# Optimization experiments

Measured on AMD Instinct MI355X. Metric: run time of the kernel, lower is better.

The kernel has to match this reference:

```python
import jax, jax.numpy as jnp
import numpy as np

N = 100000
E = 1600000
IN_DIM = 128
HEADS = 8
OUT_PER_HEAD = 16  # output_dim // heads = 128 // 8
NEG_SLOPE = 0.2    # PyG GATConv default negative_slope


def setup_inputs() -> dict:
    key = jax.random.key(0)
    k_x, k_ei, k_w, k_as, k_ad, k_b = jax.random.split(key, 6)
    x = jax.random.normal(k_x, (N, IN_DIM), dtype=jnp.float32)
    edge_index = jax.random.randint(k_ei, (2, E), 0, N, dtype=jnp.int64)
    # GATConv params (Glorot-ish scale)
    scale = 1.0 / np.sqrt(IN_DIM)
    W = jax.random.normal(k_w, (IN_DIM, HEADS, OUT_PER_HEAD), dtype=jnp.float32) * scale
    a_src = jax.random.normal(k_as, (HEADS, OUT_PER_HEAD), dtype=jnp.float32) * scale
    a_dst = jax.random.normal(k_ad, (HEADS, OUT_PER_HEAD), dtype=jnp.float32) * scale
    bias = jnp.zeros((HEADS * OUT_PER_HEAD,), dtype=jnp.float32)
    return {"x": x, "edge_index": edge_index, "W": W, "a_src": a_src,
            "a_dst": a_dst, "bias": bias}


def reference(x, edge_index, W, a_src, a_dst, bias):
    # Linear projection per head: [N, H, F]
    xp = jnp.einsum('ni,ihf->nhf', x, W)
    # Per-node attention halves: [N, H]
    al_src = jnp.einsum('nhf,hf->nh', xp, a_src)
    al_dst = jnp.einsum('nhf,hf->nh', xp, a_dst)
    src, dst = edge_index[0], edge_index[1]
    # Edge logits with LeakyReLU: [E, H]
    e = al_src[src] + al_dst[dst]
    e = jnp.where(e >= 0, e, NEG_SLOPE * e)
    # Segment softmax over incoming edges of each dst node
    m = jnp.full((N, HEADS), -jnp.inf, dtype=e.dtype).at[dst].max(e)
    ex = jnp.exp(e - m[dst])
    denom = jnp.zeros((N, HEADS), dtype=e.dtype).at[dst].add(ex)
    alpha = ex / jnp.where(denom[dst] == 0, 1.0, denom[dst])  # [E, H]
    # Weighted scatter-aggregate of source messages: [N, H, F]
    out = jnp.zeros((N, HEADS, OUT_PER_HEAD), dtype=xp.dtype)
    out = out.at[dst].add(xp[src] * alpha[:, :, None])
    # Concat heads, bias, ELU (GATLayer applies F.elu)
    out = out.reshape(N, HEADS * OUT_PER_HEAD) + bias
    return jnp.where(out > 0, out, jnp.expm1(out))
```

## Files before the change

kernel.cpp:

```cpp
#include <hip/hip_runtime.h>
#include <hip/hip_fp16.h>
#include <cstdint>

constexpr int IN_DIM = 128;
constexpr int OUT_DIM = 128;
constexpr int HEADS = 8;
constexpr float NEG_SLOPE = 0.2f;

constexpr int BUCKET_CAP = 5120;
constexpr int BIN_TILE   = 4096;

typedef _Float16 f16x8 __attribute__((ext_vector_type(8)));
typedef float    f32x4 __attribute__((ext_vector_type(4)));

__global__ __launch_bounds__(256) void proj_kernel(
    const float* __restrict__ x, const float* __restrict__ W,
    __half* __restrict__ xp, int N)
{
  __shared__ __half xs[64 * 128];
  __shared__ __half Wt[128 * 128];
  const int t  = threadIdx.x;
  const int r0 = blockIdx.x * 64;

#pragma unroll
  for (int it = 0; it < 4; ++it) {
    int m   = t + it * 256;
    int row = m >> 4;
    int g   = m & 15;
    int grow = r0 + row;
    float4 v0 = make_float4(0.f,0.f,0.f,0.f), v1 = v0;
    if (grow < N) {
      const float* src = &x[(size_t)grow * IN_DIM + g * 8];
      v0 = *(const float4*)src;
      v1 = *(const float4*)(src + 4);
    }
    union { __half2 h2[4]; uint4 u; } u;
    u.h2[0] = __floats2half2_rn(v0.x, v0.y);
    u.h2[1] = __floats2half2_rn(v0.z, v0.w);
    u.h2[2] = __floats2half2_rn(v1.x, v1.y);
    u.h2[3] = __floats2half2_rn(v1.z, v1.w);
    *(uint4*)&xs[row * 128 + ((g ^ (row & 15)) << 3)] = u.u;
  }
#pragma unroll
  for (int it = 0; it < 16; ++it) {
    int m  = t + it * 256;
    int c  = m & 127;
    int kq = m >> 7;
    int k  = kq * 4;
    float w0 = W[(size_t)(k + 0) * OUT_DIM + c];
    float w1 = W[(size_t)(k + 1) * OUT_DIM + c];
    float w2 = W[(size_t)(k + 2) * OUT_DIM + c];
    float w3 = W[(size_t)(k + 3) * OUT_DIM + c];
    union { __half2 h2[2]; uint2 u; } u;
    u.h2[0] = __floats2half2_rn(w0, w1);
    u.h2[1] = __floats2half2_rn(w2, w3);
    int g = k >> 3;
    *(uint2*)&Wt[c * 128 + (((g ^ (c & 15)) << 3) + (k & 7))] = u.u;
  }
  __syncthreads();

  const int wv = t >> 6;
  const int l  = t & 63;
  const int fr = l & 15;
  const int fq = l >> 4;

  f32x4 acc[8];
#pragma unroll
  for (int ct = 0; ct < 8; ++ct) acc[ct] = (f32x4){0.f,0.f,0.f,0.f};

#pragma unroll
  for (int ks = 0; ks < 4; ++ks) {
    int g = 4 * ks + fq;
    f16x8 a = *(const f16x8*)&xs[(16 * wv + fr) * 128 + ((g ^ fr) << 3)];
#pragma unroll
    for (int ct = 0; ct < 8; ++ct) {
      f16x8 b = *(const f16x8*)&Wt[(16 * ct + fr) * 128 + ((g ^ fr) << 3)];
      acc[ct] = __builtin_amdgcn_mfma_f32_16x16x32_f16(a, b, acc[ct], 0, 0, 0);
    }
  }
  __syncthreads();

#pragma unroll
  for (int ct = 0; ct < 8; ++ct)
#pragma unroll
    for (int r = 0; r < 4; ++r)
      xs[(16 * wv + 4 * fq + r) * 128 + 16 * ct + fr] = __float2half(acc[ct][r]);
  __syncthreads();

#pragma unroll
  for (int it = 0; it < 4; ++it) {
    int m   = t + it * 256;
    int row = m >> 4;
    int u4  = m & 15;
    int grow = r0 + row;
    if (grow < N) {
      uint4 v = *(const uint4*)&xs[row * 128 + u4 * 8];
      *(uint4*)&xp[(size_t)grow * OUT_DIM + u4 * 8] = v;
    }
  }
}

__global__ __launch_bounds__(256) void att_kernel(
    const __half* __restrict__ xp, const float* __restrict__ a_src,
    const float* __restrict__ a_dst, float* __restrict__ als,
    float* __restrict__ ald, int N)
{
  int node = blockIdx.x * 4 + (threadIdx.x >> 6);
  if (node >= N) return;
  const int l = threadIdx.x & 63;
  float2 f  = __half22float2(*(const __half2*)&xp[(size_t)node * OUT_DIM + 2 * l]);
  float2 as = *(const float2*)&a_src[2 * l];
  float2 ad = *(const float2*)&a_dst[2 * l];
  float sp = f.x * as.x + f.y * as.y;
  float dp = f.x * ad.x + f.y * ad.y;
  sp += __shfl_xor(sp, 1); sp += __shfl_xor(sp, 2); sp += __shfl_xor(sp, 4);
  dp += __shfl_xor(dp, 1); dp += __shfl_xor(dp, 2); dp += __shfl_xor(dp, 4);
  if ((l & 7) == 0) {
    als[node * HEADS + (l >> 3)] = sp;
    ald[node * HEADS + (l >> 3)] = dp;
  }
}

__global__ void detect_kernel(const void* __restrict__ ei, int E, int N,
                              int* __restrict__ flag) {
  const long long* e64 = (const long long*)ei;
  int lane = threadIdx.x;
  int step = E > 64 ? E / 64 : 1;
  size_t idx = ((size_t)lane * step) % (size_t)E;
  long long v = e64[idx];
  int bad = (v < 0 || v >= (long long)N) ? 1 : 0;
  unsigned long long m = __ballot(bad);
  if (lane == 0) *flag = (m == 0ull) ? 1 : 0;
}

__device__ __forceinline__ int load_idx(const void* ei, size_t i, int is64) {
  return is64 ? (int)((const long long*)ei)[i] : ((const int*)ei)[i];
}

__global__ __launch_bounds__(256) void bin_kernel(
    const void* __restrict__ ei, const int* __restrict__ flag,
    int* __restrict__ bucket_cnt, unsigned int* __restrict__ buckets,
    int E)
{
  __shared__ int cnt[512];
  const int is64 = *flag;
  const int t = threadIdx.x;
  cnt[t] = 0; cnt[t + 256] = 0;
  __syncthreads();

  unsigned int rec[16];
  short bk[16];
  const int base_e = blockIdx.x * BIN_TILE;
#pragma unroll
  for (int j = 0; j < 16; ++j) {
    int idx = base_e + j * 256 + t;
    bk[j] = -1;
    if (idx < E) {
      int s = load_idx(ei, (size_t)idx, is64);
      int d = load_idx(ei, (size_t)E + idx, is64);
      rec[j] = ((unsigned)(d & 255) << 24) | (unsigned)s;
      bk[j] = (short)(d >> 8);
      atomicAdd(&cnt[d >> 8], 1);
    }
  }
  __syncthreads();

  int c0 = cnt[t];
  cnt[t] = (c0 > 0) ? atomicAdd(&bucket_cnt[t], c0) : 0;
  int c1 = cnt[t + 256];
  cnt[t + 256] = (c1 > 0) ? atomicAdd(&bucket_cnt[t + 256], c1) : 0;
  __syncthreads();

#pragma unroll
  for (int j = 0; j < 16; ++j) {
    if (bk[j] >= 0) {
      int pos = atomicAdd(&cnt[bk[j]], 1);
      if (pos < BUCKET_CAP)
        buckets[(size_t)bk[j] * BUCKET_CAP + pos] = rec[j];
    }
  }
}

__global__ __launch_bounds__(512) void bucket_scan(const int* __restrict__ bucket_cnt,
                                                   int* __restrict__ bucket_base) {
  __shared__ int lds[512];
  int t = threadIdx.x;
  int v = bucket_cnt[t];
  lds[t] = v;
  __syncthreads();
  for (int d = 1; d < 512; d <<= 1) {
    int u = (t >= d) ? lds[t - d] : 0;
    __syncthreads();
    lds[t] += u;
    __syncthreads();
  }
  bucket_base[t] = lds[t] - v;
  if (t == 511) bucket_base[512] = lds[511];
}

__global__ __launch_bounds__(256) void sort_bucket(
    const unsigned int* __restrict__ buckets, const int* __restrict__ bucket_base,
    int* __restrict__ csr, int* __restrict__ row_off, int N, int E)
{
  __shared__ unsigned int recs[BUCKET_CAP];
  __shared__ int cnt[256];
  __shared__ int sc[256];
  const int b = blockIdx.x;
  const int t = threadIdx.x;
  const int base = bucket_base[b];
  int m = bucket_base[b + 1] - base;
  if (m > BUCKET_CAP) m = BUCKET_CAP;

  cnt[t] = 0;
  __syncthreads();
  for (int i = t; i < m; i += 256) {
    unsigned int r = buckets[(size_t)b * BUCKET_CAP + i];
    recs[i] = r;
    atomicAdd(&cnt[r >> 24], 1);
  }
  __syncthreads();

  sc[t] = cnt[t];
  __syncthreads();
  for (int d = 1; d < 256; d <<= 1) {
    int u = (t >= d) ? sc[t - d] : 0;
    __syncthreads();
    sc[t] += u;
    __syncthreads();
  }
  int excl = sc[t] - cnt[t];

  int n = (b << 8) + t;
  if (n < N) row_off[n] = base + excl;
  if (b == 0 && t == 0) row_off[N] = E;

  cnt[t] = base + excl;
  __syncthreads();
  for (int i = t; i < m; i += 256) {
    unsigned int r = recs[i];
    int pos = atomicAdd(&cnt[r >> 24], 1);
    csr[pos] = (int)(r & 0x00FFFFFFu);
  }
}

__global__ __launch_bounds__(256) void aggregate_kernel(
    const __half* __restrict__ xp, const float* __restrict__ als,
    const float* __restrict__ ald, const int* __restrict__ row_off,
    const int* __restrict__ csr, const float* __restrict__ bias,
    float* __restrict__ out, int N)
{
  int node = blockIdx.x * 4 + (threadIdx.x >> 6);
  if (node >= N) return;
  const int lane = threadIdx.x & 63;
  const int j = lane & 7;
  const int h = lane >> 3;
  const float ad = ald[node * HEADS + h];
  int beg = row_off[node], end = row_off[node + 1];
  beg = __builtin_amdgcn_readfirstlane(beg);
  end = __builtin_amdgcn_readfirstlane(end);

  float acc0 = 0.f, acc1 = 0.f, den_p = 0.f;
  const int nfull = (end - beg) & ~7;
  const int full_end = beg + nfull;
  int i = beg;
  for (; i < full_end; i += 8) {
    int s = csr[i + j];
    float as = als[s * HEADS + h];
    float e = as + ad; e = e >= 0.f ? e : NEG_SLOPE * e;
    float w = __expf(e);
    den_p += w;
#pragma unroll
    for (int q = 0; q < 8; ++q) {
      int   sq = __shfl(s, q);
      float wq = __shfl(w, (lane & 56) | q);
      float2 f = __half22float2(*(const __half2*)&xp[(size_t)sq * OUT_DIM + 2 * lane]);
      acc0 = fmaf(wq, f.x, acc0);
      acc1 = fmaf(wq, f.y, acc1);
    }
  }
  if (i < end) {
    int rem = end - i;
    int idx = i + j;
    int s = csr[idx < end ? idx : i];
    float as = als[s * HEADS + h];
    float e = as + ad; e = e >= 0.f ? e : NEG_SLOPE * e;
    float w = (j < rem) ? __expf(e) : 0.f;
    den_p += w;
    for (int q = 0; q < rem; ++q) {
      int   sq = __shfl(s, q);
      float wq = __shfl(w, (lane & 56) | q);
      float2 f = __half22float2(*(const __half2*)&xp[(size_t)sq * OUT_DIM + 2 * lane]);
      acc0 = fmaf(wq, f.x, acc0);
      acc1 = fmaf(wq, f.y, acc1);
    }
  }
  den_p += __shfl_xor(den_p, 1);
  den_p += __shfl_xor(den_p, 2);
  den_p += __shfl_xor(den_p, 4);

  float inv = den_p > 0.f ? 1.f / den_p : 0.f;
  float2 b = *(const float2*)&bias[2 * lane];
  float v0 = fmaf(acc0, inv, b.x);
  float v1 = fmaf(acc1, inv, b.y);
  float2 o;
  o.x = v0 > 0.f ? v0 : expm1f(v0);
  o.y = v1 > 0.f ? v1 : expm1f(v1);
  *(float2*)&out[(size_t)node * OUT_DIM + 2 * lane] = o;
}

extern "C" void kernel_launch(void* const* d_in, const int* in_sizes, int n_in,
                              void* d_out, int out_size, void* d_ws, size_t ws_size,
                              hipStream_t stream) {
  const float* x      = (const float*)d_in[0];
  const void*  ei     = d_in[1];
  const float* W      = (const float*)d_in[2];
  const float* a_src  = (const float*)d_in[3];
  const float* a_dst  = (const float*)d_in[4];
  const float* bias   = (const float*)d_in[5];
  float* out = (float*)d_out;
  const int N = in_sizes[0] / IN_DIM;
  const int E = in_sizes[1] / 2;
  const int NB  = (N + 255) >> 8;
  const int nbt = (E + BIN_TILE - 1) / BIN_TILE;

  char* ws = (char*)d_ws;
  size_t off = 0;
  __half* xp          = (__half*)(ws + off); off += (size_t)N * OUT_DIM * 2;
  off = (off + 15) & ~(size_t)15;
  float* als          = (float*)(ws + off);  off += (size_t)N * HEADS * 4;
  float* ald          = (float*)(ws + off);  off += (size_t)N * HEADS * 4;
  int*   bucket_cnt   = (int*)(ws + off);    off += 512 * 4;
  int*   bucket_base  = (int*)(ws + off);    off += 516 * 4;
  unsigned int* buckets = (unsigned int*)(ws + off); off += (size_t)512 * BUCKET_CAP * 4;
  int*   csr          = (int*)(ws + off);    off += (size_t)E * 4;
  int*   row_off      = (int*)(ws + off);    off += ((size_t)N + 4) * 4;
  int*   flag         = (int*)(ws + off);    off += 16;

  hipMemsetAsync(bucket_cnt, 0, 512 * 4, stream);
  detect_kernel<<<1, 64, 0, stream>>>(ei, E, N, flag);

  proj_kernel<<<(N + 63) / 64, 256, 0, stream>>>(x, W, xp, N);
  att_kernel<<<(N + 3) / 4, 256, 0, stream>>>(xp, a_src, a_dst, als, ald, N);

  bin_kernel<<<nbt, 256, 0, stream>>>(ei, flag, bucket_cnt, buckets, E);
  bucket_scan<<<1, 512, 0, stream>>>(bucket_cnt, bucket_base);
  sort_bucket<<<NB, 256, 0, stream>>>(buckets, bucket_base, csr, row_off, N, E);
  aggregate_kernel<<<(N + 3) / 4, 256, 0, stream>>>(xp, als, ald, row_off, csr,
                                                    bias, out, N);
}
```

Baseline: 256.9 us.

## Fold attention projections into GEMM, shrink buckets, software-pipeline aggregation

Precomputes W·a_src and W·a_dst as 16 extra GEMM columns so proj_kernel emits the per-node attention logits directly, which removes att_kernel and its re-read of xp. Halves the bucket width (1024 buckets of 128 nodes, smaller bin tiles) so more blocks run the binning and sort stages. The aggregation loop now prefetches the next chunk's source indices and logits while the current chunk is being accumulated. In exchange the logits are computed from fp16-rounded weight products, bucket capacity headroom shrinks, and the scan runs with 1024 threads.

After: 257.7 us. About the same (+0.3%).

```diff
diff --git a/kernel.cpp b/kernel.cpp
--- a/kernel.cpp
+++ b/kernel.cpp
@@ -7,18 +7,38 @@
 constexpr int HEADS = 8;
 constexpr float NEG_SLOPE = 0.2f;
 
-constexpr int BUCKET_CAP = 5120;
-constexpr int BIN_TILE   = 4096;
+constexpr int BUCKET_CAP = 2560;
+constexpr int BIN_TILE   = 2048;
 
 typedef _Float16 f16x8 __attribute__((ext_vector_type(8)));
 typedef float    f32x4 __attribute__((ext_vector_type(4)));
 
+__global__ void wa_kernel(const float* __restrict__ W, const float* __restrict__ a_src,
+                          const float* __restrict__ a_dst, __half* __restrict__ wa) {
+  int k = threadIdx.x;
+  if (k < 128) {
+#pragma unroll
+    for (int h = 0; h < 8; ++h) {
+      float s = 0.f, d = 0.f;
+#pragma unroll
+      for (int f = 0; f < 16; ++f) {
+        float w = W[k * 128 + h * 16 + f];
+        s += w * a_src[h * 16 + f];
+        d += w * a_dst[h * 16 + f];
+      }
+      wa[k * 16 + h]     = __float2half(s);
+      wa[k * 16 + 8 + h] = __float2half(d);
+    }
+  }
+}
+
 __global__ __launch_bounds__(256) void proj_kernel(
     const float* __restrict__ x, const float* __restrict__ W,
-    __half* __restrict__ xp, int N)
+    const __half* __restrict__ wa, __half* __restrict__ xp,
+    float* __restrict__ als, float* __restrict__ ald, int N)
 {
   __shared__ __half xs[64 * 128];
-  __shared__ __half Wt[128 * 128];
+  __shared__ __half Wt[144 * 128];
   const int t  = threadIdx.x;
   const int r0 = blockIdx.x * 64;
 
@@ -57,6 +77,21 @@
     int g = k >> 3;
     *(uint2*)&Wt[c * 128 + (((g ^ (c & 15)) << 3) + (k & 7))] = u.u;
   }
+#pragma unroll
+  for (int it = 0; it < 2; ++it) {
+    int m  = t + it * 256;
+    int c  = m & 15;
+    int kq = m >> 4;
+    int k  = kq * 4;
+    union { __half h[4]; uint2 u; } u;
+    u.h[0] = wa[(k + 0) * 16 + c];
+    u.h[1] = wa[(k + 1) * 16 + c];
+    u.h[2] = wa[(k + 2) * 16 + c];
+    u.h[3] = wa[(k + 3) * 16 + c];
+    int cc = 128 + c;
+    int g = k >> 3;
+    *(uint2*)&Wt[cc * 128 + (((g ^ (cc & 15)) << 3) + (k & 7))] = u.u;
+  }
   __syncthreads();
 
   const int wv = t >> 6;
@@ -64,21 +99,31 @@
   const int fr = l & 15;
   const int fq = l >> 4;
 
-  f32x4 acc[8];
-#pragma unroll
-  for (int ct = 0; ct < 8; ++ct) acc[ct] = (f32x4){0.f,0.f,0.f,0.f};
+  f32x4 acc[9];
+#pragma unroll
+  for (int ct = 0; ct < 9; ++ct) acc[ct] = (f32x4){0.f,0.f,0.f,0.f};
 
 #pragma unroll
   for (int ks = 0; ks < 4; ++ks) {
     int g = 4 * ks + fq;
     f16x8 a = *(const f16x8*)&xs[(16 * wv + fr) * 128 + ((g ^ fr) << 3)];
 #pragma unroll
-    for (int ct = 0; ct < 8; ++ct) {
+    for (int ct = 0; ct < 9; ++ct) {
       f16x8 b = *(const f16x8*)&Wt[(16 * ct + fr) * 128 + ((g ^ fr) << 3)];
       acc[ct] = __builtin_amdgcn_mfma_f32_16x16x32_f16(a, b, acc[ct], 0, 0, 0);
     }
   }
   __syncthreads();
+
+#pragma unroll
+  for (int r = 0; r < 4; ++r) {
+    int grow = r0 + 16 * wv + 4 * fq + r;
+    if (grow < N) {
+      float v = acc[8][r];
+      if (fr < 8) als[grow * HEADS + fr] = v;
+      else        ald[grow * HEADS + (fr - 8)] = v;
+    }
+  }
 
 #pragma unroll
   for (int ct = 0; ct < 8; ++ct)
@@ -97,27 +142,6 @@
       uint4 v = *(const uint4*)&xs[row * 128 + u4 * 8];
       *(uint4*)&xp[(size_t)grow * OUT_DIM + u4 * 8] = v;
     }
-  }
-}
-
-__global__ __launch_bounds__(256) void att_kernel(
-    const __half* __restrict__ xp, const float* __restrict__ a_src,
-    const float* __restrict__ a_dst, float* __restrict__ als,
-    float* __restrict__ ald, int N)
-{
-  int node = blockIdx.x * 4 + (threadIdx.x >> 6);
-  if (node >= N) return;
-  const int l = threadIdx.x & 63;
-  float2 f  = __half22float2(*(const __half2*)&xp[(size_t)node * OUT_DIM + 2 * l]);
-  float2 as = *(const float2*)&a_src[2 * l];
-  float2 ad = *(const float2*)&a_dst[2 * l];
-  float sp = f.x * as.x + f.y * as.y;
-  float dp = f.x * ad.x + f.y * ad.y;
-  sp += __shfl_xor(sp, 1); sp += __shfl_xor(sp, 2); sp += __shfl_xor(sp, 4);
-  dp += __shfl_xor(dp, 1); dp += __shfl_xor(dp, 2); dp += __shfl_xor(dp, 4);
-  if ((l & 7) == 0) {
-    als[node * HEADS + (l >> 3)] = sp;
-    ald[node * HEADS + (l >> 3)] = dp;
   }
 }
 
@@ -142,37 +166,39 @@
     int* __restrict__ bucket_cnt, unsigned int* __restrict__ buckets,
     int E)
 {
-  __shared__ int cnt[512];
+  __shared__ int cnt[1024];
   const int is64 = *flag;
   const int t = threadIdx.x;
-  cnt[t] = 0; cnt[t + 256] = 0;
-  __syncthreads();
-
-  unsigned int rec[16];
-  short bk[16];
+#pragma unroll
+  for (int b = t; b < 1024; b += 256) cnt[b] = 0;
+  __syncthreads();
+
+  unsigned int rec[8];
+  short bk[8];
   const int base_e = blockIdx.x * BIN_TILE;
 #pragma unroll
-  for (int j = 0; j < 16; ++j) {
+  for (int j = 0; j < 8; ++j) {
     int idx = base_e + j * 256 + t;
     bk[j] = -1;
     if (idx < E) {
       int s = load_idx(ei, (size_t)idx, is64);
       int d = load_idx(ei, (size_t)E + idx, is64);
-      rec[j] = ((unsigned)(d & 255) << 24) | (unsigned)s;
-      bk[j] = (short)(d >> 8);
-      atomicAdd(&cnt[d >> 8], 1);
-    }
-  }
-  __syncthreads();
-
-  int c0 = cnt[t];
-  cnt[t] = (c0 > 0) ? atomicAdd(&bucket_cnt[t], c0) : 0;
-  int c1 = cnt[t + 256];
-  cnt[t + 256] = (c1 > 0) ? atomicAdd(&bucket_cnt[t + 256], c1) : 0;
-  __syncthreads();
-
-#pragma unroll
-  for (int j = 0; j < 16; ++j) {
+      rec[j] = ((unsigned)(d & 127) << 24) | (unsigned)s;
+      bk[j] = (short)(d >> 7);
+      atomicAdd(&cnt[d >> 7], 1);
+    }
+  }
+  __syncthreads();
+
+#pragma unroll
+  for (int b = t; b < 1024; b += 256) {
+    int c = cnt[b];
+    cnt[b] = (c > 0) ? atomicAdd(&bucket_cnt[b], c) : 0;
+  }
+  __syncthreads();
+
+#pragma unroll
+  for (int j = 0; j < 8; ++j) {
     if (bk[j] >= 0) {
       int pos = atomicAdd(&cnt[bk[j]], 1);
       if (pos < BUCKET_CAP)
@@ -181,21 +207,21 @@
   }
 }
 
-__global__ __launch_bounds__(512) void bucket_scan(const int* __restrict__ bucket_cnt,
-                                                   int* __restrict__ bucket_base) {
-  __shared__ int lds[512];
+__global__ __launch_bounds__(1024) void bucket_scan(const int* __restrict__ bucket_cnt,
+                                                    int* __restrict__ bucket_base) {
+  __shared__ int lds[1024];
   int t = threadIdx.x;
   int v = bucket_cnt[t];
   lds[t] = v;
   __syncthreads();
-  for (int d = 1; d < 512; d <<= 1) {
+  for (int d = 1; d < 1024; d <<= 1) {
     int u = (t >= d) ? lds[t - d] : 0;
     __syncthreads();
     lds[t] += u;
     __syncthreads();
   }
   bucket_base[t] = lds[t] - v;
-  if (t == 511) bucket_base[512] = lds[511];
+  if (t == 1023) bucket_base[1024] = lds[1023];
 }
 
 __global__ __launch_bounds__(256) void sort_bucket(
@@ -203,15 +229,15 @@
     int* __restrict__ csr, int* __restrict__ row_off, int N, int E)
 {
   __shared__ unsigned int recs[BUCKET_CAP];
-  __shared__ int cnt[256];
-  __shared__ int sc[256];
+  __shared__ int cnt[128];
+  __shared__ int sc[128];
   const int b = blockIdx.x;
   const int t = threadIdx.x;
   const int base = bucket_base[b];
   int m = bucket_base[b + 1] - base;
   if (m > BUCKET_CAP) m = BUCKET_CAP;
 
-  cnt[t] = 0;
+  if (t < 128) cnt[t] = 0;
   __syncthreads();
   for (int i = t; i < m; i += 256) {
     unsigned int r = buckets[(size_t)b * BUCKET_CAP + i];
@@ -220,21 +246,21 @@
   }
   __syncthreads();
 
-  sc[t] = cnt[t];
-  __syncthreads();
-  for (int d = 1; d < 256; d <<= 1) {
-    int u = (t >= d) ? sc[t - d] : 0;
+  if (t < 128) sc[t] = cnt[t];
+  __syncthreads();
+  for (int d = 1; d < 128; d <<= 1) {
+    int u = (t < 128 && t >= d) ? sc[t - d] : 0;
     __syncthreads();
-    sc[t] += u;
+    if (t < 128) sc[t] += u;
     __syncthreads();
   }
-  int excl = sc[t] - cnt[t];
-
-  int n = (b << 8) + t;
-  if (n < N) row_off[n] = base + excl;
+  int excl = (t < 128) ? sc[t] - cnt[t] : 0;
+
+  int n = (b << 7) + t;
+  if (t < 128 && n < N) row_off[n] = base + excl;
   if (b == 0 && t == 0) row_off[N] = E;
 
-  cnt[t] = base + excl;
+  if (t < 128) cnt[t] = base + excl;
   __syncthreads();
   for (int i = t; i < m; i += 256) {
     unsigned int r = recs[i];
@@ -260,31 +286,46 @@
   end = __builtin_amdgcn_readfirstlane(end);
 
   float acc0 = 0.f, acc1 = 0.f, den_p = 0.f;
-  const int nfull = (end - beg) & ~7;
-  const int full_end = beg + nfull;
   int i = beg;
-  for (; i < full_end; i += 8) {
-    int s = csr[i + j];
-    float as = als[s * HEADS + h];
-    float e = as + ad; e = e >= 0.f ? e : NEG_SLOPE * e;
-    float w = __expf(e);
-    den_p += w;
+  const int nfull = (end - beg) >> 3;
+  if (nfull > 0) {
+    int s_cur = csr[i + j];
+    float e0 = als[s_cur * HEADS + h] + ad;
+    float w_cur = __expf(fmaxf(e0, NEG_SLOPE * e0));
+    for (int c = 1; c < nfull; ++c) {
+      int s_nxt = csr[i + 8 + j];
+      float as_n = als[s_nxt * HEADS + h];
+      den_p += w_cur;
+#pragma unroll
+      for (int q = 0; q < 8; ++q) {
+        int   sq = __shfl(s_cur, q);
+        float wq = __shfl(w_cur, (lane & 56) | q);
+        float2 f = __half22float2(*(const __half2*)&xp[(size_t)sq * OUT_DIM + 2 * lane]);
+        acc0 = fmaf(wq, f.x, acc0);
+        acc1 = fmaf(wq, f.y, acc1);
+      }
+      float en = as_n + ad;
+      w_cur = __expf(fmaxf(en, NEG_SLOPE * en));
+      s_cur = s_nxt;
+      i += 8;
+    }
+    den_p += w_cur;
 #pragma unroll
     for (int q = 0; q < 8; ++q) {
-      int   sq = __shfl(s, q);
-      float wq = __shfl(w, (lane & 56) | q);
+      int   sq = __shfl(s_cur, q);
+      float wq = __shfl(w_cur, (lane & 56) | q);
       float2 f = __half22float2(*(const __half2*)&xp[(size_t)sq * OUT_DIM + 2 * lane]);
       acc0 = fmaf(wq, f.x, acc0);
       acc1 = fmaf(wq, f.y, acc1);
     }
+    i += 8;
   }
   if (i < end) {
     int rem = end - i;
     int idx = i + j;
     int s = csr[idx < end ? idx : i];
-    float as = als[s * HEADS + h];
-    float e = as + ad; e = e >= 0.f ? e : NEG_SLOPE * e;
-    float w = (j < rem) ? __expf(e) : 0.f;
+    float e = als[s * HEADS + h] + ad;
+    float w = (j < rem) ? __expf(fmaxf(e, NEG_SLOPE * e)) : 0.f;
     den_p += w;
     for (int q = 0; q < rem; ++q) {
       int   sq = __shfl(s, q);
@@ -320,7 +361,7 @@
   float* out = (float*)d_out;
   const int N = in_sizes[0] / IN_DIM;
   const int E = in_sizes[1] / 2;
-  const int NB  = (N + 255) >> 8;
+  const int NB  = (N + 127) >> 7;
   const int nbt = (E + BIN_TILE - 1) / BIN_TILE;
 
   char* ws = (char*)d_ws;
@@ -329,21 +370,22 @@
   off = (off + 15) & ~(size_t)15;
   float* als          = (float*)(ws + off);  off += (size_t)N * HEADS * 4;
   float* ald          = (float*)(ws + off);  off += (size_t)N * HEADS * 4;
-  int*   bucket_cnt   = (int*)(ws + off);    off += 512 * 4;
-  int*   bucket_base  = (int*)(ws + off);    off += 516 * 4;
-  unsigned int* buckets = (unsigned int*)(ws + off); off += (size_t)512 * BUCKET_CAP * 4;
+  __half* wa          = (__half*)(ws + off); off += 128 * 16 * 2;
+  int*   bucket_cnt   = (int*)(ws + off);    off += 1024 * 4;
+  int*   bucket_base  = (int*)(ws + off);    off += 1028 * 4;
+  unsigned int* buckets = (unsigned int*)(ws + off); off += (size_t)1024 * BUCKET_CAP * 4;
   int*   csr          = (int*)(ws + off);    off += (size_t)E * 4;
   int*   row_off      = (int*)(ws + off);    off += ((size_t)N + 4) * 4;
   int*   flag         = (int*)(ws + off);    off += 16;
 
-  hipMemsetAsync(bucket_cnt, 0, 512 * 4, stream);
+  hipMemsetAsync(bucket_cnt, 0, 1024 * 4, stream);
   detect_kernel<<<1, 64, 0, stream>>>(ei, E, N, flag);
-
-  proj_kernel<<<(N + 63) / 64, 256, 0, stream>>>(x, W, xp, N);
-  att_kernel<<<(N + 3) / 4, 256, 0, stream>>>(xp, a_src, a_dst, als, ald, N);
+  wa_kernel<<<1, 128, 0, stream>>>(W, a_src, a_dst, wa);
+
+  proj_kernel<<<(N + 63) / 64, 256, 0, stream>>>(x, W, wa, xp, als, ald, N);
 
   bin_kernel<<<nbt, 256, 0, stream>>>(ei, flag, bucket_cnt, buckets, E);
-  bucket_scan<<<1, 512, 0, stream>>>(bucket_cnt, bucket_base);
+  bucket_scan<<<1, 1024, 0, stream>>>(bucket_cnt, bucket_base);
   sort_bucket<<<NB, 256, 0, stream>>>(buckets, bucket_base, csr, row_off, N, E);
   aggregate_kernel<<<(N + 3) / 4, 256, 0, stream>>>(xp, als, ald, row_off, csr,
                                                     bias, out, N);
```
